# Performance work log

Measured on AMD Instinct MI355X. Metric: run time of the kernel, lower is better.

Reference implementation:

```python
import jax, jax.numpy as jnp
import numpy as np

N = 50000      # nodes
E = 800000     # edges (avg degree 16)
IN = 256       # in_features
HD = 4         # num_heads
D = 64         # out_features per head


def setup_inputs() -> dict:
    key = jax.random.key(0)
    k1, k2, k3, k4, k5 = jax.random.split(key, 5)
    h = jax.random.normal(k1, (N, IN), dtype=jnp.float32)
    edge_index = jax.random.randint(k2, (2, E), 0, N)
    # W stored as [in_features, num_heads*out_features] (h @ W == Linear(h))
    W = jax.random.normal(k3, (IN, HD * D), dtype=jnp.float32) * (1.0 / np.sqrt(IN))
    a_src = jax.random.normal(k4, (HD, D), dtype=jnp.float32) * 0.1
    a_dst = jax.random.normal(k5, (HD, D), dtype=jnp.float32) * 0.1
    return {"h": h, "edge_index": edge_index, "W": W, "a_src": a_src, "a_dst": a_dst}


def reference(h, edge_index, W, a_src, a_dst):
    n = h.shape[0]
    src, dst = edge_index[0], edge_index[1]
    # project: [N, H, D]
    hp = (h @ W).reshape(n, HD, D)
    # per-edge attention logits [E, H]
    e_src = jnp.einsum('ehd,hd->eh', hp[src], a_src)
    e_dst = jnp.einsum('ehd,hd->eh', hp[dst], a_dst)
    e = jax.nn.leaky_relu(e_src + e_dst, negative_slope=0.2)
    # segment softmax over incoming edges of each dst node
    e_max = jax.ops.segment_max(e, dst, num_segments=n)          # [N, H]
    ex = jnp.exp(e - e_max[dst])                                  # [E, H]
    e_sum = jax.ops.segment_sum(ex, dst, num_segments=n)         # [N, H]
    alpha = ex / (e_sum[dst] + 1e-16)                             # [E, H]
    # weighted aggregation
    msg = hp[src] * alpha[..., None]                              # [E, H, D]
    out = jax.ops.segment_sum(msg, dst, num_segments=n)          # [N, H, D]
    return out.reshape(n, HD * D)                                 # concat=True
```

## Files before the change

### kernel.cpp

```cpp
#include <hip/hip_runtime.h>

#define HD 4
#define D 64
#define NHD 256
#define N_IN 256
#define NPB 128

typedef __attribute__((ext_vector_type(8))) __bf16 bf16x8;
typedef __attribute__((ext_vector_type(4))) __bf16 bf16x4;
typedef __attribute__((ext_vector_type(4))) float f32x4;

constexpr int AROW = 40;

__global__ __launch_bounds__(256) void pre_kernel(const float* __restrict__ W,
                                                  __bf16* __restrict__ Wt,
                                                  const int* __restrict__ ei,
                                                  int* __restrict__ deg8, int Nn, int E) {
  const int b = blockIdx.x;
  if (b < N_IN) {
    const int k = b, n = threadIdx.x;
    Wt[n * N_IN + k] = (__bf16)W[k * NHD + n];
  } else {
    const int e = (b - N_IN) * 256 + threadIdx.x;
    const int c = b & 7;
    if (e < E) atomicAdd(&deg8[c * Nn + ei[E + e]], 1);
  }
}

__global__ __launch_bounds__(256) void gemm_scan_kernel(
    const float* __restrict__ A, const __bf16* __restrict__ Wt,
    const float* __restrict__ a_src, const float* __restrict__ a_dst,
    __bf16* __restrict__ hp16, float* __restrict__ s_out, float* __restrict__ t_out,
    int M, const int* __restrict__ deg8, int* __restrict__ partial8,
    int* __restrict__ blocksum8, int NB, int MT) {
  __shared__ __bf16 As[128 * AROW];
  __shared__ __bf16 Bs[128 * AROW];
  __shared__ int ws4[4];
  const int tid = threadIdx.x;

  if ((int)blockIdx.x < NB) {
    const int lane = tid & 63, wv = tid >> 6;
    const int base = blockIdx.x * 1024 + tid * 4;
#pragma unroll 1
    for (int c = 0; c < 8; ++c) {
      int v0 = 0, v1 = 0, v2 = 0, v3 = 0;
      if (base + 3 < M) {
        int4 q = *(const int4*)&deg8[c * M + base];
        v0 = q.x; v1 = q.y; v2 = q.z; v3 = q.w;
      } else {
        if (base + 0 < M) v0 = deg8[c * M + base + 0];
        if (base + 1 < M) v1 = deg8[c * M + base + 1];
        if (base + 2 < M) v2 = deg8[c * M + base + 2];
        if (base + 3 < M) v3 = deg8[c * M + base + 3];
      }
      const int sum = v0 + v1 + v2 + v3;
      int incl = sum;
#pragma unroll
      for (int off = 1; off < 64; off <<= 1) {
        int y = __shfl_up(incl, off);
        if (lane >= off) incl += y;
      }
      if (lane == 63) ws4[wv] = incl;
      __syncthreads();
      int wbase = 0;
#pragma unroll
      for (int w = 0; w < 4; ++w)
        if (w < wv) wbase += ws4[w];
      __syncthreads();
      const int excl = wbase + incl - sum;
      if (base + 0 < M) partial8[c * M + base + 0] = excl;
      if (base + 1 < M) partial8[c * M + base + 1] = excl + v0;
      if (base + 2 < M) partial8[c * M + base + 2] = excl + v0 + v1;
      if (base + 3 < M) partial8[c * M + base + 3] = excl + v0 + v1 + v2;
      if (tid == 255) blocksum8[c * NB + blockIdx.x] = wbase + incl;
    }
    return;
  }

  const int g = blockIdx.x - NB;
  const int bx = g % MT, by = g / MT;
  const int lane = tid & 63, wv = tid >> 6;
  const int wr = wv >> 1, wc = wv & 1;
  const int c15 = lane & 15, quad = lane >> 4;
  const int m0 = bx * 128, n0 = by * 128;

  f32x4 acc[4][4];
#pragma unroll
  for (int i = 0; i < 4; ++i)
#pragma unroll
    for (int j = 0; j < 4; ++j) acc[i][j] = (f32x4){0.f, 0.f, 0.f, 0.f};

  const int am = tid >> 1, aks = (tid & 1) * 16;
  const int gr = m0 + am;
  const bool arow_ok = (gr < M);
  const float* Arow = &A[(size_t)gr * N_IN];
  const __bf16* Brow = &Wt[(size_t)(n0 + am) * N_IN];

  for (int kc = 0; kc < 8; ++kc) {
    const int k0 = kc * 32;
    float4 f0, f1, f2, f3;
    if (arow_ok) {
      f0 = *(const float4*)&Arow[k0 + aks + 0];
      f1 = *(const float4*)&Arow[k0 + aks + 4];
      f2 = *(const float4*)&Arow[k0 + aks + 8];
      f3 = *(const float4*)&Arow[k0 + aks + 12];
    } else {
      f0 = f1 = f2 = f3 = make_float4(0.f, 0.f, 0.f, 0.f);
    }
    bf16x8 b0 = *(const bf16x8*)&Brow[k0 + aks];
    bf16x8 b1 = *(const bf16x8*)&Brow[k0 + aks + 8];

    __syncthreads();
    bf16x8 a0, a1;
    a0[0] = (__bf16)f0.x; a0[1] = (__bf16)f0.y; a0[2] = (__bf16)f0.z; a0[3] = (__bf16)f0.w;
    a0[4] = (__bf16)f1.x; a0[5] = (__bf16)f1.y; a0[6] = (__bf16)f1.z; a0[7] = (__bf16)f1.w;
    a1[0] = (__bf16)f2.x; a1[1] = (__bf16)f2.y; a1[2] = (__bf16)f2.z; a1[3] = (__bf16)f2.w;
    a1[4] = (__bf16)f3.x; a1[5] = (__bf16)f3.y; a1[6] = (__bf16)f3.z; a1[7] = (__bf16)f3.w;
    *(bf16x8*)&As[am * AROW + aks + 0] = a0;
    *(bf16x8*)&As[am * AROW + aks + 8] = a1;
    *(bf16x8*)&Bs[am * AROW + aks + 0] = b0;
    *(bf16x8*)&Bs[am * AROW + aks + 8] = b1;
    __syncthreads();

    bf16x8 af[4], bf_[4];
#pragma unroll
    for (int i = 0; i < 4; ++i) {
      af[i]  = *(bf16x8*)&As[(wr * 64 + i * 16 + c15) * AROW + quad * 8];
      bf_[i] = *(bf16x8*)&Bs[(wc * 64 + i * 16 + c15) * AROW + quad * 8];
    }
#pragma unroll
    for (int mi = 0; mi < 4; ++mi)
#pragma unroll
      for (int ni = 0; ni < 4; ++ni)
        acc[mi][ni] = __builtin_amdgcn_mfma_f32_16x16x32_bf16(af[mi], bf_[ni], acc[mi][ni], 0, 0, 0);
  }

  const int head = by * 2 + wc;
  float av[4], ad[4];
#pragma unroll
  for (int ni = 0; ni < 4; ++ni) {
    av[ni] = a_src[head * D + ni * 16 + c15];
    ad[ni] = a_dst[head * D + ni * 16 + c15];
  }
  const int row0w = m0 + wr * 64;
#pragma unroll
  for (int mi = 0; mi < 4; ++mi) {
#pragma unroll
    for (int j = 0; j < 4; ++j) {
      float ps = acc[mi][0][j] * av[0] + acc[mi][1][j] * av[1] +
                 acc[mi][2][j] * av[2] + acc[mi][3][j] * av[3];
      float pt = acc[mi][0][j] * ad[0] + acc[mi][1][j] * ad[1] +
                 acc[mi][2][j] * ad[2] + acc[mi][3][j] * ad[3];
#pragma unroll
      for (int m = 1; m < 16; m <<= 1) {
        ps += __shfl_xor(ps, m);
        pt += __shfl_xor(pt, m);
      }
      const int row = row0w + mi * 16 + quad * 4 + j;
      if (c15 == 0 && row < M) {
        s_out[row * HD + head] = ps;
        t_out[row * HD + head] = pt;
      }
    }
#pragma unroll
    for (int ni = 0; ni < 4; ++ni) {
#pragma unroll
      for (int j = 0; j < 4; ++j) {
        const int row = row0w + mi * 16 + quad * 4 + j;
        const int col = n0 + wc * 64 + ni * 16 + c15;
        if (row < M) hp16[(size_t)row * NHD + col] = (__bf16)acc[mi][ni][j];
      }
    }
  }
}

__global__ __launch_bounds__(256) void scan23_kernel(
    const int* __restrict__ partial8, const int* __restrict__ blocksum8,
    int* __restrict__ row_ptr, int* __restrict__ pcur0, int* __restrict__ cursor8,
    int n, int NB) {
  __shared__ int s_choff[8], s_B[8], s_T[8];
  const int tid = threadIdx.x;
  if (tid < 64) {
    int runB = 0;
#pragma unroll 1
    for (int c = 0; c < 8; ++c) {
      int v = (tid < NB) ? blocksum8[c * NB + tid] : 0;
      int incl = v;
#pragma unroll
      for (int off = 1; off < 64; off <<= 1) {
        int y = __shfl_up(incl, off);
        if (tid >= off) incl += y;
      }
      const int excl = incl - v;
      const int choff = __shfl(excl, (int)blockIdx.x);
      const int Tc = __shfl(incl, NB - 1);
      if (tid == 0) { s_choff[c] = choff; s_B[c] = runB; s_T[c] = Tc; }
      runB += Tc;
    }
    if (blockIdx.x == 0 && tid == 0) row_ptr[n] = runB;
  }
  __syncthreads();
  if (blockIdx.x == 0 && tid < 8)
    pcur0[tid * (n + 1) + n] = s_B[tid] + s_T[tid];
  const int base = blockIdx.x * 1024 + tid * 4;
  int rp0 = 0, rp1 = 0, rp2 = 0, rp3 = 0;
  const bool full = (base + 3 < n);
#pragma unroll 1
  for (int c = 0; c < 8; ++c) {
    int p0 = 0, p1 = 0, p2 = 0, p3 = 0;
    if (full) {
      int4 q = *(const int4*)&partial8[c * n + base];
      p0 = q.x; p1 = q.y; p2 = q.z; p3 = q.w;
    } else {
      if (base + 0 < n) p0 = partial8[c * n + base + 0];
      if (base + 1 < n) p1 = partial8[c * n + base + 1];
      if (base + 2 < n) p2 = partial8[c * n + base + 2];
    }
    const int ch = s_choff[c], bB = s_B[c];
    if (base + 0 < n) { int P = ch + p0, pc = bB + P; pcur0[c*(n+1)+base+0] = pc; cursor8[c*n+base+0] = pc; rp0 += P; }
    if (base + 1 < n) { int P = ch + p1, pc = bB + P; pcur0[c*(n+1)+base+1] = pc; cursor8[c*n+base+1] = pc; rp1 += P; }
    if (base + 2 < n) { int P = ch + p2, pc = bB + P; pcur0[c*(n+1)+base+2] = pc; cursor8[c*n+base+2] = pc; rp2 += P; }
    if (base + 3 < n) { int P = ch + p3, pc = bB + P; pcur0[c*(n+1)+base+3] = pc; cursor8[c*n+base+3] = pc; rp3 += P; }
  }
  if (base + 0 < n) row_ptr[base + 0] = rp0;
  if (base + 1 < n) row_ptr[base + 1] = rp1;
  if (base + 2 < n) row_ptr[base + 2] = rp2;
  if (base + 3 < n) row_ptr[base + 3] = rp3;
}

__global__ void scatter_kernel(const int* __restrict__ ei, int* __restrict__ cursor8,
                               int* __restrict__ tmp_src, int Nn, int E) {
  int e = blockIdx.x * blockDim.x + threadIdx.x;
  if (e >= E) return;
  const int c = blockIdx.x & 7;
  int sn = ei[e], dn = ei[E + e];
  int pos = atomicAdd(&cursor8[c * Nn + dn], 1);
  tmp_src[pos] = sn;
}

__global__ __launch_bounds__(256) void permute_kernel(
    const int* __restrict__ pcur0, const int* __restrict__ row_ptr,
    const int* __restrict__ tmp_src, int* __restrict__ csr_src, int n) {
  __shared__ int spc[8][NPB + 1];
  __shared__ int sO[8][NPB];
  __shared__ int srp[NPB];
  const int tid = threadIdx.x;
  const int n0 = blockIdx.x * NPB;
  const int cnt = (n - n0 < NPB) ? (n - n0) : NPB;
  for (int idx = tid; idx < 8 * (NPB + 1); idx += 256) {
    const int c = idx / (NPB + 1), i = idx - c * (NPB + 1);
    int ni = n0 + i; if (ni > n) ni = n;
    spc[c][i] = pcur0[c * (n + 1) + ni];
  }
  for (int i = tid; i < cnt; i += 256) srp[i] = row_ptr[n0 + i];
  __syncthreads();
  for (int i = tid; i < cnt; i += 256) {
    int run = 0;
#pragma unroll
    for (int c = 0; c < 8; ++c) { sO[c][i] = run; run += spc[c][i + 1] - spc[c][i]; }
  }
  __syncthreads();
  const int lane = tid & 63, wv = tid >> 6;
#pragma unroll 1
  for (int c = wv; c < 8; c += 4) {
    const int S = spc[c][0];
    const int L = spc[c][cnt] - S;
    for (int k = lane; k < L; k += 64) {
      const int q = S + k;
      const int val = tmp_src[q];
      int lo = 0, hi = cnt;
      while (hi - lo > 1) {
        const int mid = (lo + hi) >> 1;
        if (spc[c][mid] <= q) lo = mid; else hi = mid;
      }
      const int dest = srp[lo] + sO[c][lo] + (q - spc[c][lo]);
      csr_src[dest] = val;
    }
  }
}

__global__ __launch_bounds__(256) void aggregate_kernel(
    const int* __restrict__ row_ptr, const int* __restrict__ csr_src,
    const float* __restrict__ s, const float* __restrict__ t,
    const __bf16* __restrict__ hp16, float* __restrict__ out, int N) {
  const int wave = threadIdx.x >> 6;
  const int lane = threadIdx.x & 63;
  const int node = blockIdx.x * 4 + wave;
  if (node >= N) return;
  const int h = lane >> 4;
  const int d0 = lane * 4;
  const int beg = row_ptr[node], end = row_ptr[node + 1];
  const float tn = t[node * HD + h];
  float num0 = 0.f, num1 = 0.f, num2 = 0.f, num3 = 0.f, den = 0.f;
  int i = beg;
  for (; i + 4 <= end; i += 4) {
    int sn0 = csr_src[i], sn1 = csr_src[i + 1], sn2 = csr_src[i + 2], sn3 = csr_src[i + 3];
    bf16x4 v0 = *(const bf16x4*)&hp16[(size_t)sn0 * NHD + d0];
    bf16x4 v1 = *(const bf16x4*)&hp16[(size_t)sn1 * NHD + d0];
    bf16x4 v2 = *(const bf16x4*)&hp16[(size_t)sn2 * NHD + d0];
    bf16x4 v3 = *(const bf16x4*)&hp16[(size_t)sn3 * NHD + d0];
    float lg0 = s[sn0 * HD + h] + tn;
    float lg1 = s[sn1 * HD + h] + tn;
    float lg2 = s[sn2 * HD + h] + tn;
    float lg3 = s[sn3 * HD + h] + tn;
    lg0 = fmaxf(lg0, 0.2f * lg0);
    lg1 = fmaxf(lg1, 0.2f * lg1);
    lg2 = fmaxf(lg2, 0.2f * lg2);
    lg3 = fmaxf(lg3, 0.2f * lg3);
    float ex0 = __expf(lg0), ex1 = __expf(lg1), ex2 = __expf(lg2), ex3 = __expf(lg3);
    den += (ex0 + ex1) + (ex2 + ex3);
    num0 += ex0 * (float)v0[0] + ex1 * (float)v1[0] + ex2 * (float)v2[0] + ex3 * (float)v3[0];
    num1 += ex0 * (float)v0[1] + ex1 * (float)v1[1] + ex2 * (float)v2[1] + ex3 * (float)v3[1];
    num2 += ex0 * (float)v0[2] + ex1 * (float)v1[2] + ex2 * (float)v2[2] + ex3 * (float)v3[2];
    num3 += ex0 * (float)v0[3] + ex1 * (float)v1[3] + ex2 * (float)v2[3] + ex3 * (float)v3[3];
  }
  for (; i < end; ++i) {
    int sn0 = csr_src[i];
    bf16x4 v0 = *(const bf16x4*)&hp16[(size_t)sn0 * NHD + d0];
    float lg0 = s[sn0 * HD + h] + tn;
    lg0 = fmaxf(lg0, 0.2f * lg0);
    float ex0 = __expf(lg0);
    den += ex0;
    num0 += ex0 * (float)v0[0];
    num1 += ex0 * (float)v0[1];
    num2 += ex0 * (float)v0[2];
    num3 += ex0 * (float)v0[3];
  }
  const float inv = 1.0f / (den + 1e-16f);
  float4 o = make_float4(num0 * inv, num1 * inv, num2 * inv, num3 * inv);
  *(float4*)&out[(size_t)node * NHD + d0] = o;
}

extern "C" void kernel_launch(void* const* d_in, const int* in_sizes, int n_in,
                              void* d_out, int out_size, void* d_ws, size_t ws_size,
                              hipStream_t stream) {
  const float* h_ptr  = (const float*)d_in[0];
  const int*   ei     = (const int*)d_in[1];
  const float* W      = (const float*)d_in[2];
  const float* a_src  = (const float*)d_in[3];
  const float* a_dst  = (const float*)d_in[4];
  float* out = (float*)d_out;

  const int N = in_sizes[0] / N_IN;
  const int E = in_sizes[1] / 2;
  const int NB = (N + 1023) / 1024;
  const int MT = (N + 127) / 128;

  auto align256 = [](size_t x) { return (x + 255) & ~size_t(255); };
  char* base = (char*)d_ws;
  size_t off = 0;
  __bf16* hp16 = (__bf16*)(base + off);  off += align256((size_t)N * NHD * 2);
  __bf16* Wt   = (__bf16*)(base + off);  off += align256((size_t)N_IN * NHD * 2);
  float* s        = (float*)(base + off); off += align256((size_t)N * HD * 4);
  float* t        = (float*)(base + off); off += align256((size_t)N * HD * 4);
  int*   deg8     = (int*)(base + off);   off += align256((size_t)N * 8 * 4);
  int*   cursor8  = (int*)(base + off);   off += align256((size_t)N * 8 * 4);
  int*   partial8 = (int*)(base + off);   off += align256((size_t)N * 8 * 4);
  int*   blocksum8= (int*)(base + off);   off += align256((size_t)NB * 8 * 4);
  int*   row_ptr  = (int*)(base + off);   off += align256((size_t)(N + 1) * 4);
  int*   pcur0    = (int*)(base + off);   off += align256((size_t)(N + 1) * 8 * 4);
  int*   tmp_src  = (int*)(base + off);   off += align256((size_t)E * 4);
  int*   csr_src  = (int*)(base + off);   off += align256((size_t)E * 4);

  hipMemsetAsync(deg8, 0, (size_t)N * 8 * 4, stream);
  pre_kernel<<<N_IN + (E + 255) / 256, 256, 0, stream>>>(W, Wt, ei, deg8, N, E);
  gemm_scan_kernel<<<NB + MT * 2, 256, 0, stream>>>(h_ptr, Wt, a_src, a_dst,
                                                    hp16, s, t, N, deg8, partial8,
                                                    blocksum8, NB, MT);
  scan23_kernel<<<NB, 256, 0, stream>>>(partial8, blocksum8, row_ptr, pcur0, cursor8, N, NB);
  scatter_kernel<<<(E + 255) / 256, 256, 0, stream>>>(ei, cursor8, tmp_src, N, E);
  permute_kernel<<<(N + NPB - 1) / NPB, 256, 0, stream>>>(pcur0, row_ptr, tmp_src, csr_src, N);
  aggregate_kernel<<<(N + 3) / 4, 256, 0, stream>>>(row_ptr, csr_src, s, t, hp16, out, N);
}
```

Before: 282.9 us.

## Fuse CSR build and aggregation into persistent cooperative kernels with grid syncs

Replaces the memset plus preprocessing kernel with one cooperative kernel that zeroes the degree counters, does a grid-wide sync, then transposes W and counts degrees. The scan, scatter, permute and aggregate kernels are merged into a single persistent cooperative kernel whose grid-stride phases are separated by grid.sync(). This removes several launches and inter-kernel gaps. In exchange the grid size is capped by occupancy, the aggregation phase runs with fewer resident blocks than before, and every grid-wide barrier adds a stall.

```diff
diff --git a/kernel.cpp b/kernel.cpp
--- a/kernel.cpp
+++ b/kernel.cpp
@@ -1,4 +1,7 @@
 #include <hip/hip_runtime.h>
+#include <hip/hip_cooperative_groups.h>
+
+namespace cg = cooperative_groups;
 
 #define HD 4
 #define D 64
@@ -12,18 +15,24 @@
 
 constexpr int AROW = 40;
 
-__global__ __launch_bounds__(256) void pre_kernel(const float* __restrict__ W,
-                                                  __bf16* __restrict__ Wt,
-                                                  const int* __restrict__ ei,
-                                                  int* __restrict__ deg8, int Nn, int E) {
-  const int b = blockIdx.x;
-  if (b < N_IN) {
-    const int k = b, n = threadIdx.x;
-    Wt[n * N_IN + k] = (__bf16)W[k * NHD + n];
-  } else {
-    const int e = (b - N_IN) * 256 + threadIdx.x;
-    const int c = b & 7;
-    if (e < E) atomicAdd(&deg8[c * Nn + ei[E + e]], 1);
+__global__ __launch_bounds__(256) void preA_kernel(const float* __restrict__ W,
+                                                   __bf16* __restrict__ Wt,
+                                                   const int* __restrict__ ei,
+                                                   int* __restrict__ deg8,
+                                                   int Nn, int E, int NCH) {
+  cg::grid_group grid = cg::this_grid();
+  const int tid = threadIdx.x;
+  const int gsz = gridDim.x;
+  for (int idx = blockIdx.x * 256 + tid; idx < Nn * 8; idx += gsz * 256) deg8[idx] = 0;
+  grid.sync();
+  for (int chunk = blockIdx.x; chunk < NCH; chunk += gsz) {
+    if (chunk < N_IN) {
+      Wt[tid * N_IN + chunk] = (__bf16)W[chunk * NHD + tid];
+    } else {
+      const int e = (chunk - N_IN) * 256 + tid;
+      const int c = chunk & 7;
+      if (e < E) atomicAdd(&deg8[c * Nn + ei[E + e]], 1);
+    }
   }
 }
 
@@ -174,161 +183,171 @@
   }
 }
 
-__global__ __launch_bounds__(256) void scan23_kernel(
+__global__ __launch_bounds__(256) void csr_agg_kernel(
     const int* __restrict__ partial8, const int* __restrict__ blocksum8,
     int* __restrict__ row_ptr, int* __restrict__ pcur0, int* __restrict__ cursor8,
-    int n, int NB) {
-  __shared__ int s_choff[8], s_B[8], s_T[8];
+    const int* __restrict__ ei, int* __restrict__ tmp_src, int* __restrict__ csr_src,
+    const float* __restrict__ s, const float* __restrict__ t,
+    const __bf16* __restrict__ hp16, float* __restrict__ out,
+    int n, int E, int NB) {
+  cg::grid_group grid = cg::this_grid();
+  __shared__ union {
+    struct { int choff[8]; int B[8]; int T[8]; } sc;
+    struct { int spc[8][NPB + 1]; int sO[8][NPB]; int srp[NPB]; } pm;
+  } sh;
   const int tid = threadIdx.x;
-  if (tid < 64) {
-    int runB = 0;
+  const int gsz = gridDim.x;
+
+  for (int chunk = blockIdx.x; chunk < NB; chunk += gsz) {
+    if (tid < 64) {
+      int runB = 0;
+#pragma unroll 1
+      for (int c = 0; c < 8; ++c) {
+        int v = (tid < NB) ? blocksum8[c * NB + tid] : 0;
+        int incl = v;
+#pragma unroll
+        for (int off = 1; off < 64; off <<= 1) {
+          int y = __shfl_up(incl, off);
+          if (tid >= off) incl += y;
+        }
+        const int excl = incl - v;
+        const int choff = __shfl(excl, chunk);
+        const int Tc = __shfl(incl, NB - 1);
+        if (tid == 0) { sh.sc.choff[c] = choff; sh.sc.B[c] = runB; sh.sc.T[c] = Tc; }
+        runB += Tc;
+      }
+      if (chunk == 0 && tid == 0) row_ptr[n] = runB;
+    }
+    __syncthreads();
+    if (chunk == 0 && tid < 8)
+      pcur0[tid * (n + 1) + n] = sh.sc.B[tid] + sh.sc.T[tid];
+    const int base = chunk * 1024 + tid * 4;
+    int rp0 = 0, rp1 = 0, rp2 = 0, rp3 = 0;
+    const bool full = (base + 3 < n);
 #pragma unroll 1
     for (int c = 0; c < 8; ++c) {
-      int v = (tid < NB) ? blocksum8[c * NB + tid] : 0;
-      int incl = v;
-#pragma unroll
-      for (int off = 1; off < 64; off <<= 1) {
-        int y = __shfl_up(incl, off);
-        if (tid >= off) incl += y;
-      }
-      const int excl = incl - v;
-      const int choff = __shfl(excl, (int)blockIdx.x);
-      const int Tc = __shfl(incl, NB - 1);
-      if (tid == 0) { s_choff[c] = choff; s_B[c] = runB; s_T[c] = Tc; }
-      runB += Tc;
-    }
-    if (blockIdx.x == 0 && tid == 0) row_ptr[n] = runB;
-  }
-  __syncthreads();
-  if (blockIdx.x == 0 && tid < 8)
-    pcur0[tid * (n + 1) + n] = s_B[tid] + s_T[tid];
-  const int base = blockIdx.x * 1024 + tid * 4;
-  int rp0 = 0, rp1 = 0, rp2 = 0, rp3 = 0;
-  const bool full = (base + 3 < n);
+      int p0 = 0, p1 = 0, p2 = 0, p3 = 0;
+      if (full) {
+        int4 q = *(const int4*)&partial8[c * n + base];
+        p0 = q.x; p1 = q.y; p2 = q.z; p3 = q.w;
+      } else {
+        if (base + 0 < n) p0 = partial8[c * n + base + 0];
+        if (base + 1 < n) p1 = partial8[c * n + base + 1];
+        if (base + 2 < n) p2 = partial8[c * n + base + 2];
+      }
+      const int ch = sh.sc.choff[c], bB = sh.sc.B[c];
+      if (base + 0 < n) { int P = ch + p0, pc = bB + P; pcur0[c*(n+1)+base+0] = pc; cursor8[c*n+base+0] = pc; rp0 += P; }
+      if (base + 1 < n) { int P = ch + p1, pc = bB + P; pcur0[c*(n+1)+base+1] = pc; cursor8[c*n+base+1] = pc; rp1 += P; }
+      if (base + 2 < n) { int P = ch + p2, pc = bB + P; pcur0[c*(n+1)+base+2] = pc; cursor8[c*n+base+2] = pc; rp2 += P; }
+      if (base + 3 < n) { int P = ch + p3, pc = bB + P; pcur0[c*(n+1)+base+3] = pc; cursor8[c*n+base+3] = pc; rp3 += P; }
+    }
+    if (base + 0 < n) row_ptr[base + 0] = rp0;
+    if (base + 1 < n) row_ptr[base + 1] = rp1;
+    if (base + 2 < n) row_ptr[base + 2] = rp2;
+    if (base + 3 < n) row_ptr[base + 3] = rp3;
+    __syncthreads();
+  }
+  grid.sync();
+
+  const int ECH = (E + 255) >> 8;
+  for (int ec = blockIdx.x; ec < ECH; ec += gsz) {
+    const int e = ec * 256 + tid;
+    if (e < E) {
+      const int c = ec & 7;
+      int sn = ei[e], dn = ei[E + e];
+      int pos = atomicAdd(&cursor8[c * n + dn], 1);
+      tmp_src[pos] = sn;
+    }
+  }
+  grid.sync();
+
+  const int PNB = (n + NPB - 1) / NPB;
+  for (int pb = blockIdx.x; pb < PNB; pb += gsz) {
+    __syncthreads();
+    const int n0 = pb * NPB;
+    const int cnt = (n - n0 < NPB) ? (n - n0) : NPB;
+    for (int idx = tid; idx < 8 * (NPB + 1); idx += 256) {
+      const int c = idx / (NPB + 1), i2 = idx - c * (NPB + 1);
+      int ni = n0 + i2; if (ni > n) ni = n;
+      sh.pm.spc[c][i2] = pcur0[c * (n + 1) + ni];
+    }
+    for (int i2 = tid; i2 < cnt; i2 += 256) sh.pm.srp[i2] = row_ptr[n0 + i2];
+    __syncthreads();
+    for (int i2 = tid; i2 < cnt; i2 += 256) {
+      int run = 0;
+#pragma unroll
+      for (int c = 0; c < 8; ++c) { sh.pm.sO[c][i2] = run; run += sh.pm.spc[c][i2 + 1] - sh.pm.spc[c][i2]; }
+    }
+    __syncthreads();
+    const int lane = tid & 63, wv = tid >> 6;
 #pragma unroll 1
-  for (int c = 0; c < 8; ++c) {
-    int p0 = 0, p1 = 0, p2 = 0, p3 = 0;
-    if (full) {
-      int4 q = *(const int4*)&partial8[c * n + base];
-      p0 = q.x; p1 = q.y; p2 = q.z; p3 = q.w;
-    } else {
-      if (base + 0 < n) p0 = partial8[c * n + base + 0];
-      if (base + 1 < n) p1 = partial8[c * n + base + 1];
-      if (base + 2 < n) p2 = partial8[c * n + base + 2];
-    }
-    const int ch = s_choff[c], bB = s_B[c];
-    if (base + 0 < n) { int P = ch + p0, pc = bB + P; pcur0[c*(n+1)+base+0] = pc; cursor8[c*n+base+0] = pc; rp0 += P; }
-    if (base + 1 < n) { int P = ch + p1, pc = bB + P; pcur0[c*(n+1)+base+1] = pc; cursor8[c*n+base+1] = pc; rp1 += P; }
-    if (base + 2 < n) { int P = ch + p2, pc = bB + P; pcur0[c*(n+1)+base+2] = pc; cursor8[c*n+base+2] = pc; rp2 += P; }
-    if (base + 3 < n) { int P = ch + p3, pc = bB + P; pcur0[c*(n+1)+base+3] = pc; cursor8[c*n+base+3] = pc; rp3 += P; }
-  }
-  if (base + 0 < n) row_ptr[base + 0] = rp0;
-  if (base + 1 < n) row_ptr[base + 1] = rp1;
-  if (base + 2 < n) row_ptr[base + 2] = rp2;
-  if (base + 3 < n) row_ptr[base + 3] = rp3;
-}
-
-__global__ void scatter_kernel(const int* __restrict__ ei, int* __restrict__ cursor8,
-                               int* __restrict__ tmp_src, int Nn, int E) {
-  int e = blockIdx.x * blockDim.x + threadIdx.x;
-  if (e >= E) return;
-  const int c = blockIdx.x & 7;
-  int sn = ei[e], dn = ei[E + e];
-  int pos = atomicAdd(&cursor8[c * Nn + dn], 1);
-  tmp_src[pos] = sn;
-}
-
-__global__ __launch_bounds__(256) void permute_kernel(
-    const int* __restrict__ pcur0, const int* __restrict__ row_ptr,
-    const int* __restrict__ tmp_src, int* __restrict__ csr_src, int n) {
-  __shared__ int spc[8][NPB + 1];
-  __shared__ int sO[8][NPB];
-  __shared__ int srp[NPB];
-  const int tid = threadIdx.x;
-  const int n0 = blockIdx.x * NPB;
-  const int cnt = (n - n0 < NPB) ? (n - n0) : NPB;
-  for (int idx = tid; idx < 8 * (NPB + 1); idx += 256) {
-    const int c = idx / (NPB + 1), i = idx - c * (NPB + 1);
-    int ni = n0 + i; if (ni > n) ni = n;
-    spc[c][i] = pcur0[c * (n + 1) + ni];
-  }
-  for (int i = tid; i < cnt; i += 256) srp[i] = row_ptr[n0 + i];
-  __syncthreads();
-  for (int i = tid; i < cnt; i += 256) {
-    int run = 0;
-#pragma unroll
-    for (int c = 0; c < 8; ++c) { sO[c][i] = run; run += spc[c][i + 1] - spc[c][i]; }
-  }
-  __syncthreads();
-  const int lane = tid & 63, wv = tid >> 6;
-#pragma unroll 1
-  for (int c = wv; c < 8; c += 4) {
-    const int S = spc[c][0];
-    const int L = spc[c][cnt] - S;
-    for (int k = lane; k < L; k += 64) {
-      const int q = S + k;
-      const int val = tmp_src[q];
-      int lo = 0, hi = cnt;
-      while (hi - lo > 1) {
-        const int mid = (lo + hi) >> 1;
-        if (spc[c][mid] <= q) lo = mid; else hi = mid;
-      }
-      const int dest = srp[lo] + sO[c][lo] + (q - spc[c][lo]);
-      csr_src[dest] = val;
-    }
-  }
-}
-
-__global__ __launch_bounds__(256) void aggregate_kernel(
-    const int* __restrict__ row_ptr, const int* __restrict__ csr_src,
-    const float* __restrict__ s, const float* __restrict__ t,
-    const __bf16* __restrict__ hp16, float* __restrict__ out, int N) {
-  const int wave = threadIdx.x >> 6;
-  const int lane = threadIdx.x & 63;
-  const int node = blockIdx.x * 4 + wave;
-  if (node >= N) return;
+    for (int c = wv; c < 8; c += 4) {
+      const int S = sh.pm.spc[c][0];
+      const int L = sh.pm.spc[c][cnt] - S;
+      for (int k = lane; k < L; k += 64) {
+        const int q = S + k;
+        const int val = tmp_src[q];
+        int lo = 0, hi = cnt;
+        while (hi - lo > 1) {
+          const int mid = (lo + hi) >> 1;
+          if (sh.pm.spc[c][mid] <= q) lo = mid; else hi = mid;
+        }
+        const int dest = sh.pm.srp[lo] + sh.pm.sO[c][lo] + (q - sh.pm.spc[c][lo]);
+        csr_src[dest] = val;
+      }
+    }
+  }
+  grid.sync();
+
+  const int NG = (n + 3) >> 2;
+  const int wave = tid >> 6;
+  const int lane = tid & 63;
   const int h = lane >> 4;
   const int d0 = lane * 4;
-  const int beg = row_ptr[node], end = row_ptr[node + 1];
-  const float tn = t[node * HD + h];
-  float num0 = 0.f, num1 = 0.f, num2 = 0.f, num3 = 0.f, den = 0.f;
-  int i = beg;
-  for (; i + 4 <= end; i += 4) {
-    int sn0 = csr_src[i], sn1 = csr_src[i + 1], sn2 = csr_src[i + 2], sn3 = csr_src[i + 3];
-    bf16x4 v0 = *(const bf16x4*)&hp16[(size_t)sn0 * NHD + d0];
-    bf16x4 v1 = *(const bf16x4*)&hp16[(size_t)sn1 * NHD + d0];
-    bf16x4 v2 = *(const bf16x4*)&hp16[(size_t)sn2 * NHD + d0];
-    bf16x4 v3 = *(const bf16x4*)&hp16[(size_t)sn3 * NHD + d0];
-    float lg0 = s[sn0 * HD + h] + tn;
-    float lg1 = s[sn1 * HD + h] + tn;
-    float lg2 = s[sn2 * HD + h] + tn;
-    float lg3 = s[sn3 * HD + h] + tn;
-    lg0 = fmaxf(lg0, 0.2f * lg0);
-    lg1 = fmaxf(lg1, 0.2f * lg1);
-    lg2 = fmaxf(lg2, 0.2f * lg2);
-    lg3 = fmaxf(lg3, 0.2f * lg3);
-    float ex0 = __expf(lg0), ex1 = __expf(lg1), ex2 = __expf(lg2), ex3 = __expf(lg3);
-    den += (ex0 + ex1) + (ex2 + ex3);
-    num0 += ex0 * (float)v0[0] + ex1 * (float)v1[0] + ex2 * (float)v2[0] + ex3 * (float)v3[0];
-    num1 += ex0 * (float)v0[1] + ex1 * (float)v1[1] + ex2 * (float)v2[1] + ex3 * (float)v3[1];
-    num2 += ex0 * (float)v0[2] + ex1 * (float)v1[2] + ex2 * (float)v2[2] + ex3 * (float)v3[2];
-    num3 += ex0 * (float)v0[3] + ex1 * (float)v1[3] + ex2 * (float)v2[3] + ex3 * (float)v3[3];
-  }
-  for (; i < end; ++i) {
-    int sn0 = csr_src[i];
-    bf16x4 v0 = *(const bf16x4*)&hp16[(size_t)sn0 * NHD + d0];
-    float lg0 = s[sn0 * HD + h] + tn;
-    lg0 = fmaxf(lg0, 0.2f * lg0);
-    float ex0 = __expf(lg0);
-    den += ex0;
-    num0 += ex0 * (float)v0[0];
-    num1 += ex0 * (float)v0[1];
-    num2 += ex0 * (float)v0[2];
-    num3 += ex0 * (float)v0[3];
-  }
-  const float inv = 1.0f / (den + 1e-16f);
-  float4 o = make_float4(num0 * inv, num1 * inv, num2 * inv, num3 * inv);
-  *(float4*)&out[(size_t)node * NHD + d0] = o;
+  for (int g2 = blockIdx.x; g2 < NG; g2 += gsz) {
+    const int node = g2 * 4 + wave;
+    if (node >= n) continue;
+    const int beg = row_ptr[node], end = row_ptr[node + 1];
+    const float tn = t[node * HD + h];
+    float num0 = 0.f, num1 = 0.f, num2 = 0.f, num3 = 0.f, den = 0.f;
+    int i = beg;
+    for (; i + 4 <= end; i += 4) {
+      int sn0 = csr_src[i], sn1 = csr_src[i + 1], sn2 = csr_src[i + 2], sn3 = csr_src[i + 3];
+      bf16x4 v0 = *(const bf16x4*)&hp16[(size_t)sn0 * NHD + d0];
+      bf16x4 v1 = *(const bf16x4*)&hp16[(size_t)sn1 * NHD + d0];
+      bf16x4 v2 = *(const bf16x4*)&hp16[(size_t)sn2 * NHD + d0];
+      bf16x4 v3 = *(const bf16x4*)&hp16[(size_t)sn3 * NHD + d0];
+      float lg0 = s[sn0 * HD + h] + tn;
+      float lg1 = s[sn1 * HD + h] + tn;
+      float lg2 = s[sn2 * HD + h] + tn;
+      float lg3 = s[sn3 * HD + h] + tn;
+      lg0 = fmaxf(lg0, 0.2f * lg0);
+      lg1 = fmaxf(lg1, 0.2f * lg1);
+      lg2 = fmaxf(lg2, 0.2f * lg2);
+      lg3 = fmaxf(lg3, 0.2f * lg3);
+      float ex0 = __expf(lg0), ex1 = __expf(lg1), ex2 = __expf(lg2), ex3 = __expf(lg3);
+      den += (ex0 + ex1) + (ex2 + ex3);
+      num0 += ex0 * (float)v0[0] + ex1 * (float)v1[0] + ex2 * (float)v2[0] + ex3 * (float)v3[0];
+      num1 += ex0 * (float)v0[1] + ex1 * (float)v1[1] + ex2 * (float)v2[1] + ex3 * (float)v3[1];
+      num2 += ex0 * (float)v0[2] + ex1 * (float)v1[2] + ex2 * (float)v2[2] + ex3 * (float)v3[2];
+      num3 += ex0 * (float)v0[3] + ex1 * (float)v1[3] + ex2 * (float)v2[3] + ex3 * (float)v3[3];
+    }
+    for (; i < end; ++i) {
+      int sn0 = csr_src[i];
+      bf16x4 v0 = *(const bf16x4*)&hp16[(size_t)sn0 * NHD + d0];
+      float lg0 = s[sn0 * HD + h] + tn;
+      lg0 = fmaxf(lg0, 0.2f * lg0);
+      float ex0 = __expf(lg0);
+      den += ex0;
+      num0 += ex0 * (float)v0[0];
+      num1 += ex0 * (float)v0[1];
+      num2 += ex0 * (float)v0[2];
+      num3 += ex0 * (float)v0[3];
+    }
+    const float inv = 1.0f / (den + 1e-16f);
+    float4 o = make_float4(num0 * inv, num1 * inv, num2 * inv, num3 * inv);
+    *(float4*)&out[(size_t)node * NHD + d0] = o;
+  }
 }
 
 extern "C" void kernel_launch(void* const* d_in, const int* in_sizes, int n_in,
@@ -345,6 +364,7 @@
   const int E = in_sizes[1] / 2;
   const int NB = (N + 1023) / 1024;
   const int MT = (N + 127) / 128;
+  const int NCH = N_IN + (E + 255) / 256;
 
   auto align256 = [](size_t x) { return (x + 255) & ~size_t(255); };
   char* base = (char*)d_ws;
@@ -362,13 +382,36 @@
   int*   tmp_src  = (int*)(base + off);   off += align256((size_t)E * 4);
   int*   csr_src  = (int*)(base + off);   off += align256((size_t)E * 4);
 
-  hipMemsetAsync(deg8, 0, (size_t)N * 8 * 4, stream);
-  pre_kernel<<<N_IN + (E + 255) / 256, 256, 0, stream>>>(W, Wt, ei, deg8, N, E);
+  static int gridA = 0, gridC = 0;
+  if (!gridA) {
+    int pa = 0, pc = 0;
+    if (hipOccupancyMaxActiveBlocksPerMultiprocessor(&pa, preA_kernel, 256, 0) != hipSuccess || pa < 1) pa = 4;
+    if (hipOccupancyMaxActiveBlocksPerMultiprocessor(&pc, csr_agg_kernel, 256, 0) != hipSuccess || pc < 1) pc = 4;
+    if (pa > 8) pa = 8;
+    if (pc > 8) pc = 8;
+    gridA = ((pa * 256) / 8) * 8;
+    gridC = ((pc * 256) / 8) * 8;
+    if (gridA < 8) gridA = 8;
+    if (gridC < 8) gridC = 8;
+  }
+
+  {
+    const float* W_ = W; __bf16* Wt_ = Wt; const int* ei_ = ei; int* dg_ = deg8;
+    int N_ = N, E_ = E, NCH_ = NCH;
+    void* args[] = {&W_, &Wt_, &ei_, &dg_, &N_, &E_, &NCH_};
+    hipLaunchCooperativeKernel(preA_kernel, dim3(gridA), dim3(256), args, 0, stream);
+  }
   gemm_scan_kernel<<<NB + MT * 2, 256, 0, stream>>>(h_ptr, Wt, a_src, a_dst,
                                                     hp16, s, t, N, deg8, partial8,
                                                     blocksum8, NB, MT);
-  scan23_kernel<<<NB, 256, 0, stream>>>(partial8, blocksum8, row_ptr, pcur0, cursor8, N, NB);
-  scatter_kernel<<<(E + 255) / 256, 256, 0, stream>>>(ei, cursor8, tmp_src, N, E);
-  permute_kernel<<<(N + NPB - 1) / NPB, 256, 0, stream>>>(pcur0, row_ptr, tmp_src, csr_src, N);
-  aggregate_kernel<<<(N + 3) / 4, 256, 0, stream>>>(row_ptr, csr_src, s, t, hp16, out, N);
+  {
+    const int* pa8 = partial8; const int* bs8 = blocksum8;
+    int* rp_ = row_ptr; int* pc0 = pcur0; int* cu8 = cursor8;
+    const int* ei_ = ei; int* tsrc = tmp_src; int* csrc = csr_src;
+    const float* s_ = s; const float* t_ = t; const __bf16* hp_ = hp16;
+    float* out_ = out; int N_ = N, E_ = E, NB_ = NB;
+    void* args[] = {&pa8, &bs8, &rp_, &pc0, &cu8, &ei_, &tsrc, &csrc,
+                    &s_, &t_, &hp_, &out_, &N_, &E_, &NB_};
+    hipLaunchCooperativeKernel(csr_agg_kernel, dim3(gridC), dim3(256), args, 0, stream);
+  }
 }
```

Result: slower. 733.1 us (+159.1%).
